# Optimization experiments

Hardware: AMD Instinct MI355X
Metric: run time of the kernel (lower is better)

Reference implementation:

```python
import jax, jax.numpy as jnp
import numpy as np

EMBED_DIM = 512
NUM_HEADS = 8
WINDOW = 5
OVERLAP = 1
STRIDE = WINDOW - OVERLAP  # 4


def setup_inputs() -> dict:
    key = jax.random.key(0)
    ks = jax.random.split(key, 5)
    B, S, D = 8, 4096, EMBED_DIM
    s = 1.0 / np.sqrt(D).astype(np.float32)
    return {
        "x": jax.random.normal(ks[0], (B, S, D), jnp.float32),
        "Wq": jax.random.normal(ks[1], (D, D), jnp.float32) * s,
        "bq": jnp.zeros((D,), jnp.float32),
        "Wk": jax.random.normal(ks[2], (D, D), jnp.float32) * s,
        "bk": jnp.zeros((D,), jnp.float32),
        "Wv": jax.random.normal(ks[3], (D, D), jnp.float32) * s,
        "bv": jnp.zeros((D,), jnp.float32),
        "Wo": jax.random.normal(ks[4], (D, D), jnp.float32) * s,
        "bo": jnp.zeros((D,), jnp.float32),
    }


def reference(x, Wq, bq, Wk, bk, Wv, bv, Wo, bo):
    B, S, D = x.shape
    H = NUM_HEADS
    hd = D // H
    pad = (WINDOW - S % WINDOW) % WINDOW
    xp = jnp.pad(x, ((0, 0), (0, pad), (0, 0)))
    P = S + pad
    nw = (P - WINDOW) // STRIDE + 1

    # gather all sliding windows at once: [B, nw, W, D]
    idx = (jnp.arange(nw) * STRIDE)[:, None] + jnp.arange(WINDOW)  # [nw, W]
    win = xp[:, idx]

    def proj(t, W, b):
        return (t @ W + b).reshape(B, nw, WINDOW, H, hd)

    q = proj(win, Wq, bq)
    k = proj(win, Wk, bk)
    v = proj(win, Wv, bv)

    scale = jnp.float32(1.0 / np.sqrt(hd))
    scores = jnp.einsum('bnqhd,bnkhd->bnhqk', q, k) * scale  # [B,nw,H,W,W]
    attn = jax.nn.softmax(scores, axis=-1)
    o = jnp.einsum('bnhqk,bnkhd->bnqhd', attn, v).reshape(B, nw, WINDOW, D)
    o = o @ Wo + bo  # window outputs [B,nw,W,D]

    # overlap-add + count-average (exactly as the torch loop does)
    flat_idx = idx.reshape(-1)
    out = jnp.zeros((B, P, D), jnp.float32).at[:, flat_idx].add(
        o.reshape(B, nw * WINDOW, D))
    counts = jnp.zeros((P,), jnp.float32).at[flat_idx].add(1.0)
    out = out / (counts[None, :, None] + 1e-6)
    out = out[:, :S]

    # torch: sum(all_weights) / num_windows  -> mean over window axis
    attn_weights = attn.mean(axis=1)  # [B, H, W, W]
    return out, attn_weights
```

## Files before the change

kernel.cpp:

```cpp
#include <hip/hip_runtime.h>
#include <hip/hip_bf16.h>


#define SEQ   4096
#define NB    8
#define DIM   512
#define NWIN  1024
#define MTOT  (NB*SEQ)

typedef __bf16 bf16x8 __attribute__((ext_vector_type(8)));
typedef float  f32x4  __attribute__((ext_vector_type(4)));

__device__ __forceinline__ float b2f(unsigned short u) {
  union { unsigned int i; float f; } z; z.i = ((unsigned int)u) << 16; return z.f;
}
__device__ __forceinline__ unsigned short f2b(float f) {
  __bf16 h = (__bf16)f; return __builtin_bit_cast(unsigned short, h);
}
__device__ __forceinline__ void gload_lds16(const void* g, void* l) {
  __builtin_amdgcn_global_load_lds(
      (__attribute__((address_space(1))) void*)g,
      (__attribute__((address_space(3))) void*)l, 16, 0, 0);
}

#define FENCE() asm volatile("" ::: "memory")
#define BAR()   __builtin_amdgcn_s_barrier()
#define LGK0()  asm volatile("s_waitcnt lgkmcnt(0)" ::: "memory")
#define SCHB()  __builtin_amdgcn_sched_barrier(0)
#define VMW4()  asm volatile("s_waitcnt vmcnt(4)" ::: "memory")
#define VMW0()  asm volatile("s_waitcnt vmcnt(0)" ::: "memory")

__global__ __launch_bounds__(256) void cvt_x(const float* __restrict__ x,
                                             unsigned short* __restrict__ o, int n8) {
  int stride = gridDim.x * blockDim.x;
  for (int i = blockIdx.x * blockDim.x + threadIdx.x; i < n8; i += stride) {
    const float4 a = *(const float4*)(x + (size_t)i * 8);
    const float4 c = *(const float4*)(x + (size_t)i * 8 + 4);
    unsigned short u[8] = {f2b(a.x), f2b(a.y), f2b(a.z), f2b(a.w),
                           f2b(c.x), f2b(c.y), f2b(c.z), f2b(c.w)};
    *(int4*)(o + (size_t)i * 8) = *(const int4*)u;
  }
}

__global__ __launch_bounds__(256) void cvt_w(const float* __restrict__ W0, const float* __restrict__ W1,
                                             const float* __restrict__ W2, const float* __restrict__ W3,
                                             unsigned short* __restrict__ Wt) {
  int i = blockIdx.x * 256 + threadIdx.x;
  int w = i >> 18;
  int r = i & 262143;
  int nn = r >> 9, kk = r & 511;
  const float* W = (w == 0) ? W0 : (w == 1) ? W1 : (w == 2) ? W2 : W3;
  Wt[i] = f2b(W[kk * 512 + nn]);
}

__device__ __forceinline__ void stage_part(int h, const unsigned short* pa, const unsigned short* pb,
    int r0s, int c0s, int r1s, int c1s, char* ldsb, int wid) {
  int kt = h >> 2, slot = (h + 2) & 3;
  int buf = kt & 1, ab = slot >> 1, half = slot & 1;
  const unsigned short* src = ab ? pb : pa;
  int rb = half << 7;
  int kc = kt << 6;
  char* d = ldsb + buf * 65536 + ab * 32768 + half * 16384 + wid * 1024;
  gload_lds16(src + (size_t)(rb + r0s) * 512 + kc + c0s, d);
  gload_lds16(src + (size_t)(rb + r1s) * 512 + kc + c1s, d + 8192);
}

#define LDSB(off) (*(const bf16x8*)(ldsb + (off)))

#define RA4(BUF, HALF) { \
  _Pragma("unroll") for (int mf2 = 0; mf2 < 4; ++mf2) { \
    _Pragma("unroll") for (int ks = 0; ks < 2; ++ks) \
      a[mf2][ks] = LDSB(aS[BUF][ks] + (HALF) * 8192 + mf2 * 2048); } }

#define RB2(BUF, QN) { \
  _Pragma("unroll") for (int nf2 = 0; nf2 < 2; ++nf2) { \
    _Pragma("unroll") for (int ks = 0; ks < 2; ++ks) \
      b[(QN)*2+nf2][ks] = LDSB(bS[BUF][ks] + (QN) * 4096 + nf2 * 2048); } }

#define MMQ(QM, QN) { \
  _Pragma("unroll") for (int ks = 0; ks < 2; ++ks) \
  _Pragma("unroll") for (int mf2 = 0; mf2 < 4; ++mf2) \
  _Pragma("unroll") for (int nf2 = 0; nf2 < 2; ++nf2) \
    acc[(QM)*4+mf2][(QN)*2+nf2] = __builtin_amdgcn_mfma_f32_16x16x32_bf16( \
      a[mf2][ks], b[(QN)*2+nf2][ks], acc[(QM)*4+mf2][(QN)*2+nf2], 0, 0, 0); }

template<int MODE>
__global__ __launch_bounds__(512, 2) void gemm8(
    const unsigned short* __restrict__ A, const unsigned short* __restrict__ Bw,
    const float* __restrict__ b0, const float* __restrict__ b1, const float* __restrict__ b2,
    unsigned short* __restrict__ o0, unsigned short* __restrict__ o1, unsigned short* __restrict__ o2,
    float* __restrict__ fout) {
  __shared__ unsigned short lds_[65536];
  char* ldsb = (char*)lds_;

  const int nwg = gridDim.x;
  const int cpx = nwg >> 3;
  const int g = blockIdx.x;
  const int sw = (g & 7) * cpx + (g >> 3);
  constexpr int NTN = (MODE == 0) ? 6 : 2;
  const int ntile = sw % NTN, mtile = sw / NTN;
  const int m0 = mtile * 256, n0g = ntile * 256;

  const int tid = threadIdx.x;
  const int lane = tid & 63;
  const int wid = tid >> 6;
  const int wr = wid >> 2, wc = wid & 3;
  const int cl16 = lane & 15, hi = lane >> 4;
  const int hi16 = hi * 16;
  const int sxor = (cl16 & 14) << 3;

  int o0_ = tid * 16;
  int o1_ = 8192 + tid * 16;
  int l0 = o0_ ^ (((o0_ >> 8) & 7) << 4);
  int l1 = o1_ ^ (((o1_ >> 8) & 7) << 4);
  const int r0s = l0 >> 7, c0s = (l0 & 127) >> 1;
  const int r1s = l1 >> 7, c1s = (l1 & 127) >> 1;

  const unsigned short* pa = A + (size_t)m0 * 512;
  const unsigned short* pb = Bw + (size_t)n0g * 512;

  int aS[2][2], bS[2][2];
#pragma unroll
  for (int bu = 0; bu < 2; ++bu)
#pragma unroll
    for (int ks = 0; ks < 2; ++ks) {
      aS[bu][ks] = bu * 65536 + ((wr * 16384 + cl16 * 128 + ks * 64 + hi16) ^ sxor);
      bS[bu][ks] = bu * 65536 + 32768 + (((wc >> 1) * 16384 + (wc & 1) * 8192 + cl16 * 128 + ks * 64 + hi16) ^ sxor);
    }

  f32x4 acc[8][4] = {};
  bf16x8 a[4][2], b[4][2];

#define STG(H) stage_part((H), pa, pb, r0s, c0s, r1s, c1s, ldsb, wid)

  STG(0); STG(1); STG(2); STG(3); STG(4); STG(5);
  VMW4();
  FENCE(); BAR();

#pragma unroll
  for (int it = 0; it < 4; ++it) {
    const int hb = 8 * it;
    RA4(0, 0); RB2(0, 0);
    STG(hb + 6);
    FENCE(); BAR(); LGK0(); SCHB();
    __builtin_amdgcn_s_setprio(1); MMQ(0, 0); __builtin_amdgcn_s_setprio(0);
    FENCE(); BAR();
    RB2(0, 1);
    if (hb + 7 < 32) STG(hb + 7);
    FENCE(); BAR(); LGK0(); SCHB();
    __builtin_amdgcn_s_setprio(1); MMQ(0, 1); __builtin_amdgcn_s_setprio(0);
    FENCE(); BAR();
    RA4(0, 1);
    if (it < 3) STG(hb + 8);
    FENCE(); BAR(); LGK0(); SCHB();
    __builtin_amdgcn_s_setprio(1); MMQ(1, 1); __builtin_amdgcn_s_setprio(0);
    FENCE(); BAR();
    if (it < 3) STG(hb + 9);
    FENCE(); BAR();
    __builtin_amdgcn_s_setprio(1); MMQ(1, 0); __builtin_amdgcn_s_setprio(0);
    if (it < 3) { VMW4(); } else { VMW0(); }
    FENCE(); BAR();
    RA4(1, 0); RB2(1, 0);
    if (it < 3) STG(hb + 10);
    FENCE(); BAR(); LGK0(); SCHB();
    __builtin_amdgcn_s_setprio(1); MMQ(0, 0); __builtin_amdgcn_s_setprio(0);
    FENCE(); BAR();
    RB2(1, 1);
    if (it < 3) STG(hb + 11);
    FENCE(); BAR(); LGK0(); SCHB();
    __builtin_amdgcn_s_setprio(1); MMQ(0, 1); __builtin_amdgcn_s_setprio(0);
    FENCE(); BAR();
    RA4(1, 1);
    if (it < 3) STG(hb + 12);
    FENCE(); BAR(); LGK0(); SCHB();
    __builtin_amdgcn_s_setprio(1); MMQ(1, 1); __builtin_amdgcn_s_setprio(0);
    FENCE(); BAR();
    if (it < 3) STG(hb + 13);
    FENCE(); BAR();
    __builtin_amdgcn_s_setprio(1); MMQ(1, 0); __builtin_amdgcn_s_setprio(0);
    if (it < 3) { VMW4(); }
    FENCE(); BAR();
  }

  if constexpr (MODE == 0) {
    const int sel = n0g >> 9;
    const float* bias = (sel == 0) ? b0 : (sel == 1) ? b1 : b2;
    unsigned short* C = (sel == 0) ? o0 : (sel == 1) ? o1 : o2;
    const int lcb = (n0g & 511) + wc * 64;
    unsigned short* wlds = lds_ + wid * 8192;
#pragma unroll
    for (int mf = 0; mf < 8; ++mf)
#pragma unroll
      for (int nf = 0; nf < 4; ++nf) {
        float bv_ = bias[lcb + nf * 16 + cl16];
#pragma unroll
        for (int r = 0; r < 4; ++r) {
          int w = (mf * 16 + hi * 4 + r) * 64 + nf * 16 + cl16;
          wlds[w ^ (((w >> 7) & 7) << 3)] = f2b(acc[mf][nf][r] + bv_);
        }
      }
    LGK0();
#pragma unroll
    for (int itr = 0; itr < 16; ++itr) {
      int f = itr * 512 + lane * 8;
      int row = f >> 6, col = f & 63;
      int4 v = *(const int4*)&wlds[f ^ (((f >> 7) & 7) << 3)];
      *(int4*)(C + (size_t)(m0 + wr * 128 + row) * 512 + lcb + col) = v;
    }
  } else {
#pragma unroll
    for (int nf = 0; nf < 4; ++nf) {
      int ncol = n0g + wc * 64 + nf * 16 + cl16;
      float bv_ = b0[ncol];
#pragma unroll
      for (int mf = 0; mf < 8; ++mf) {
        int rbase = m0 + wr * 128 + mf * 16 + hi * 4;
#pragma unroll
        for (int r = 0; r < 4; ++r) {
          int row = rbase + r;
          int s = row & (SEQ - 1);
          float cnt = ((s & 3) == 0 && s > 0) ? 2.0f : 1.0f;
          fout[(size_t)row * 512 + ncol] = (acc[mf][nf][r] + cnt * bv_) / (cnt + 1e-6f);
        }
      }
    }
  }
}

__global__ __launch_bounds__(256) void attn_win(
    const unsigned short* __restrict__ Qb, const unsigned short* __restrict__ Kb,
    const unsigned short* __restrict__ Vb,
    const float* __restrict__ bq, const float* __restrict__ bk, const float* __restrict__ bv,
    unsigned short* __restrict__ yb, unsigned short* __restrict__ yext,
    float* __restrict__ abuf) {
  const int gw = blockIdx.x * 4 + (threadIdx.x >> 6);
  const int b = gw >> 10, n = gw & (NWIN - 1);
  const int lane = threadIdx.x & 63;
  const int h = lane >> 3, e = lane & 7;
  const int dbase = h * 64 + e * 8;

  float kf[5][8], vf[5][8];
#pragma unroll
  for (int j = 0; j < 5; ++j) {
    int p = 4 * n + j;
    if (p < SEQ) {
      int4 kv = *(const int4*)(Kb + ((size_t)b * SEQ + p) * DIM + dbase);
      int4 vv = *(const int4*)(Vb + ((size_t)b * SEQ + p) * DIM + dbase);
      const unsigned short* kp = (const unsigned short*)&kv;
      const unsigned short* vp = (const unsigned short*)&vv;
#pragma unroll
      for (int d = 0; d < 8; ++d) { kf[j][d] = b2f(kp[d]); vf[j][d] = b2f(vp[d]); }
    } else {
#pragma unroll
      for (int d = 0; d < 8; ++d) { kf[j][d] = bk[dbase + d]; vf[j][d] = bv[dbase + d]; }
    }
  }
  float pm[5][5];
#pragma unroll
  for (int i = 0; i < 5; ++i) {
    int p = 4 * n + i;
    float qf[8];
    if (p < SEQ) {
      int4 qv = *(const int4*)(Qb + ((size_t)b * SEQ + p) * DIM + dbase);
      const unsigned short* qp = (const unsigned short*)&qv;
#pragma unroll
      for (int d = 0; d < 8; ++d) qf[d] = b2f(qp[d]);
    } else {
#pragma unroll
      for (int d = 0; d < 8; ++d) qf[d] = bq[dbase + d];
    }
    float sr[5];
#pragma unroll
    for (int j = 0; j < 5; ++j) {
      float t = 0.f;
#pragma unroll
      for (int d = 0; d < 8; ++d) t += qf[d] * kf[j][d];
      t += __shfl_xor(t, 1);
      t += __shfl_xor(t, 2);
      t += __shfl_xor(t, 4);
      sr[j] = t * 0.125f;
    }
    float mx = sr[0];
#pragma unroll
    for (int j = 1; j < 5; ++j) mx = fmaxf(mx, sr[j]);
    float ex[5], sum = 0.f;
#pragma unroll
    for (int j = 0; j < 5; ++j) { ex[j] = expf(sr[j] - mx); sum += ex[j]; }
    float inv = 1.0f / sum;
#pragma unroll
    for (int j = 0; j < 5; ++j) pm[i][j] = ex[j] * inv;
    float o[8];
#pragma unroll
    for (int d = 0; d < 8; ++d) o[d] = 0.f;
#pragma unroll
    for (int j = 0; j < 5; ++j)
#pragma unroll
      for (int d = 0; d < 8; ++d) o[d] += pm[i][j] * vf[j][d];
    unsigned short u[8];
#pragma unroll
    for (int d = 0; d < 8; ++d) u[d] = f2b(o[d]);
    if (i < 4) {
      *(int4*)(yb + ((size_t)b * SEQ + p) * DIM + dbase) = *(const int4*)u;
    } else {
      *(int4*)(yext + ((size_t)b * NWIN + n) * DIM + dbase) = *(const int4*)u;
    }
  }
  float* ap = abuf + ((size_t)(b * NWIN + n) * 8 + h) * 25;
  if (e == 0) {
#pragma unroll
    for (int i2 = 0; i2 < 5; ++i2)
#pragma unroll
      for (int j2 = 0; j2 < 5; ++j2) ap[i2 * 5 + j2] = pm[i2][j2];
  }
}

__global__ __launch_bounds__(256) void merge_y(unsigned short* __restrict__ y,
                                               const unsigned short* __restrict__ ye) {
  int idx = blockIdx.x * 256 + threadIdx.x;
  if (idx >= 8 * 1023 * 64) return;
  int d8 = idx & 63;
  int t = idx >> 6;
  int n = t % 1023 + 1;
  int b = t / 1023;
  size_t yo = ((size_t)b * SEQ + 4 * (size_t)n) * DIM + d8 * 8;
  size_t eo = ((size_t)b * NWIN + (n - 1)) * DIM + d8 * 8;
  int4 av = *(const int4*)(y + yo);
  int4 cv = *(const int4*)(ye + eo);
  const unsigned short* ap = (const unsigned short*)&av;
  const unsigned short* cp = (const unsigned short*)&cv;
  unsigned short u[8];
#pragma unroll
  for (int j = 0; j < 8; ++j) u[j] = f2b(b2f(ap[j]) + b2f(cp[j]));
  *(int4*)(y + yo) = *(const int4*)u;
}

__global__ __launch_bounds__(256) void attn_reduce(const float* __restrict__ abuf,
                                                   float* __restrict__ out) {
  __shared__ float sm[256][25];
  int bh = blockIdx.x;
  int b = bh >> 3, h = bh & 7;
  int t = threadIdx.x;
  float loc[25];
#pragma unroll
  for (int j = 0; j < 25; ++j) loc[j] = 0.f;
  for (int n = t; n < NWIN; n += 256) {
    const float* p = abuf + ((size_t)(b * NWIN + n) * 8 + h) * 25;
#pragma unroll
    for (int j = 0; j < 25; ++j) loc[j] += p[j];
  }
#pragma unroll
  for (int j = 0; j < 25; ++j) sm[t][j] = loc[j];
  __syncthreads();
  for (int off = 128; off > 0; off >>= 1) {
    if (t < off)
#pragma unroll
      for (int j = 0; j < 25; ++j) sm[t][j] += sm[t + off][j];
    __syncthreads();
  }
  if (t < 25) out[bh * 25 + t] = sm[0][t] * (1.0f / 1024.0f);
}

extern "C" void kernel_launch(void* const* d_in, const int* in_sizes, int n_in,
                              void* d_out, int out_size, void* d_ws, size_t ws_size,
                              hipStream_t stream) {
  const float* x  = (const float*)d_in[0];
  const float* Wq = (const float*)d_in[1];
  const float* bq = (const float*)d_in[2];
  const float* Wk = (const float*)d_in[3];
  const float* bk = (const float*)d_in[4];
  const float* Wv = (const float*)d_in[5];
  const float* bv = (const float*)d_in[6];
  const float* Wo = (const float*)d_in[7];
  const float* bo = (const float*)d_in[8];
  float* out = (float*)d_out;

  char* ws = (char*)d_ws;
  unsigned short* xb   = (unsigned short*)(ws);
  unsigned short* yb   = xb;
  unsigned short* Qb   = (unsigned short*)(ws + 33554432);
  unsigned short* Kb   = (unsigned short*)(ws + 67108864);
  unsigned short* Vb   = (unsigned short*)(ws + 100663296);
  unsigned short* yext = (unsigned short*)(ws + 134217728);
  float*          abuf = (float*)(ws + 142606336);
  unsigned short* Wt   = (unsigned short*)(ws + 149159936);
  (void)ws_size; (void)in_sizes; (void)n_in; (void)out_size;

  cvt_x<<<2048, 256, 0, stream>>>(x, xb, MTOT * DIM / 8);
  cvt_w<<<4096, 256, 0, stream>>>(Wq, Wk, Wv, Wo, Wt);
  gemm8<0><<<768, 512, 0, stream>>>(xb, Wt, bq, bk, bv, Qb, Kb, Vb, nullptr);
  attn_win<<<2048, 256, 0, stream>>>(Qb, Kb, Vb, bq, bk, bv, yb, yext, abuf);
  merge_y<<<2046, 256, 0, stream>>>(yb, yext);
  gemm8<1><<<256, 512, 0, stream>>>(yb, Wt + 3 * (DIM * DIM), bo, nullptr, nullptr,
                                    nullptr, nullptr, nullptr, out);
  attn_reduce<<<64, 256, 0, stream>>>(abuf, out + (size_t)MTOT * DIM);
}
```

Before: 160.1 us.

## Replace 8-phase interleaved GEMM schedule with simple double-buffered k-tile pipeline

The GEMM main loop used a fine-grained 8-phase schedule that interleaved quarter-tile staging, LDS reads, MFMA bursts, priority bumps and many barriers. It is replaced by a plain two-buffer loop: prefetch the whole next k-tile (four stage parts), wait on vmcnt, barrier, then do all LDS reads and MFMAs for the current buffer. This drops most barriers, sched_barriers and setprio calls to cut synchronisation overhead and simplify scheduling. In exchange it gives up the finer overlap between global loads, LDS reads and MFMA work that the old schedule tried to provide.

Measured after the change: 166.7 us. 1.04x slower.

```diff
diff --git a/kernel.cpp b/kernel.cpp
--- a/kernel.cpp
+++ b/kernel.cpp
@@ -25,10 +25,9 @@
 
 #define FENCE() asm volatile("" ::: "memory")
 #define BAR()   __builtin_amdgcn_s_barrier()
+#define VMW8()  asm volatile("s_waitcnt vmcnt(8)" ::: "memory")
+#define VMW0()  asm volatile("s_waitcnt vmcnt(0)" ::: "memory")
 #define LGK0()  asm volatile("s_waitcnt lgkmcnt(0)" ::: "memory")
-#define SCHB()  __builtin_amdgcn_sched_barrier(0)
-#define VMW4()  asm volatile("s_waitcnt vmcnt(4)" ::: "memory")
-#define VMW0()  asm volatile("s_waitcnt vmcnt(0)" ::: "memory")
 
 __global__ __launch_bounds__(256) void cvt_x(const float* __restrict__ x,
                                              unsigned short* __restrict__ o, int n8) {
@@ -85,7 +84,7 @@
       a[mf2][ks], b[(QN)*2+nf2][ks], acc[(QM)*4+mf2][(QN)*2+nf2], 0, 0, 0); }
 
 template<int MODE>
-__global__ __launch_bounds__(512, 2) void gemm8(
+__global__ __launch_bounds__(512, 2) void gemm2p(
     const unsigned short* __restrict__ A, const unsigned short* __restrict__ Bw,
     const float* __restrict__ b0, const float* __restrict__ b1, const float* __restrict__ b2,
     unsigned short* __restrict__ o0, unsigned short* __restrict__ o1, unsigned short* __restrict__ o2,
@@ -131,55 +130,24 @@
   f32x4 acc[8][4] = {};
   bf16x8 a[4][2], b[4][2];
 
-#define STG(H) stage_part((H), pa, pb, r0s, c0s, r1s, c1s, ldsb, wid)
-
-  STG(0); STG(1); STG(2); STG(3); STG(4); STG(5);
-  VMW4();
-  FENCE(); BAR();
-
-#pragma unroll
-  for (int it = 0; it < 4; ++it) {
-    const int hb = 8 * it;
-    RA4(0, 0); RB2(0, 0);
-    STG(hb + 6);
-    FENCE(); BAR(); LGK0(); SCHB();
-    __builtin_amdgcn_s_setprio(1); MMQ(0, 0); __builtin_amdgcn_s_setprio(0);
-    FENCE(); BAR();
-    RB2(0, 1);
-    if (hb + 7 < 32) STG(hb + 7);
-    FENCE(); BAR(); LGK0(); SCHB();
-    __builtin_amdgcn_s_setprio(1); MMQ(0, 1); __builtin_amdgcn_s_setprio(0);
-    FENCE(); BAR();
-    RA4(0, 1);
-    if (it < 3) STG(hb + 8);
-    FENCE(); BAR(); LGK0(); SCHB();
-    __builtin_amdgcn_s_setprio(1); MMQ(1, 1); __builtin_amdgcn_s_setprio(0);
-    FENCE(); BAR();
-    if (it < 3) STG(hb + 9);
-    FENCE(); BAR();
-    __builtin_amdgcn_s_setprio(1); MMQ(1, 0); __builtin_amdgcn_s_setprio(0);
-    if (it < 3) { VMW4(); } else { VMW0(); }
-    FENCE(); BAR();
-    RA4(1, 0); RB2(1, 0);
-    if (it < 3) STG(hb + 10);
-    FENCE(); BAR(); LGK0(); SCHB();
-    __builtin_amdgcn_s_setprio(1); MMQ(0, 0); __builtin_amdgcn_s_setprio(0);
-    FENCE(); BAR();
-    RB2(1, 1);
-    if (it < 3) STG(hb + 11);
-    FENCE(); BAR(); LGK0(); SCHB();
-    __builtin_amdgcn_s_setprio(1); MMQ(0, 1); __builtin_amdgcn_s_setprio(0);
-    FENCE(); BAR();
-    RA4(1, 1);
-    if (it < 3) STG(hb + 12);
-    FENCE(); BAR(); LGK0(); SCHB();
-    __builtin_amdgcn_s_setprio(1); MMQ(1, 1); __builtin_amdgcn_s_setprio(0);
-    FENCE(); BAR();
-    if (it < 3) STG(hb + 13);
-    FENCE(); BAR();
-    __builtin_amdgcn_s_setprio(1); MMQ(1, 0); __builtin_amdgcn_s_setprio(0);
-    if (it < 3) { VMW4(); }
-    FENCE(); BAR();
+#define STG4(KT) { stage_part((KT)*4, pa, pb, r0s, c0s, r1s, c1s, ldsb, wid); \
+                   stage_part((KT)*4+1, pa, pb, r0s, c0s, r1s, c1s, ldsb, wid); \
+                   stage_part((KT)*4+2, pa, pb, r0s, c0s, r1s, c1s, ldsb, wid); \
+                   stage_part((KT)*4+3, pa, pb, r0s, c0s, r1s, c1s, ldsb, wid); }
+
+  STG4(0);
+
+#pragma unroll
+  for (int kt = 0; kt < 8; ++kt) {
+    const int bu = kt & 1;
+    if (kt < 7) { STG4(kt + 1); VMW8(); } else { VMW0(); }
+    FENCE(); BAR(); FENCE();
+    RB2(bu, 0); RB2(bu, 1);
+    RA4(bu, 0);
+    MMQ(0, 0); MMQ(0, 1);
+    RA4(bu, 1);
+    MMQ(1, 1); MMQ(1, 0);
+    FENCE(); BAR(); FENCE();
   }
 
   if constexpr (MODE == 0) {
@@ -387,10 +355,10 @@
 
   cvt_x<<<2048, 256, 0, stream>>>(x, xb, MTOT * DIM / 8);
   cvt_w<<<4096, 256, 0, stream>>>(Wq, Wk, Wv, Wo, Wt);
-  gemm8<0><<<768, 512, 0, stream>>>(xb, Wt, bq, bk, bv, Qb, Kb, Vb, nullptr);
+  gemm2p<0><<<768, 512, 0, stream>>>(xb, Wt, bq, bk, bv, Qb, Kb, Vb, nullptr);
   attn_win<<<2048, 256, 0, stream>>>(Qb, Kb, Vb, bq, bk, bv, yb, yext, abuf);
   merge_y<<<2046, 256, 0, stream>>>(yb, yext);
-  gemm8<1><<<256, 512, 0, stream>>>(yb, Wt + 3 * (DIM * DIM), bo, nullptr, nullptr,
-                                    nullptr, nullptr, nullptr, out);
+  gemm2p<1><<<256, 512, 0, stream>>>(yb, Wt + 3 * (DIM * DIM), bo, nullptr, nullptr,
+                                     nullptr, nullptr, nullptr, out);
   attn_reduce<<<64, 256, 0, stream>>>(abuf, out + (size_t)MTOT * DIM);
 }
```

## Fuse overlap merge into a new output-projection GEMM and relax QKV GEMM waits

Applied to the files above, without the earlier changes.

Drops the separate merge_y pass. A new 128x128-tile gemm_final kernel adds the extra-window rows (yext) into the A operand while loading it, then applies the bias and count-average epilogue. This removes one full read-modify-write pass over the activations and one kernel launch. The tuned gemm8 MODE 1 path is replaced by a simpler register-staged, double-read kernel that may use the tensor cores less efficiently. Separately, the explicit lgkmcnt(0) waits and sched_barriers are removed from the QKV GEMM loop so the compiler can schedule the LDS reads and MFMAs itself.

Measured after the change: 198.7 us. +24.1%, slower.

```diff
diff --git a/kernel.cpp b/kernel.cpp
--- a/kernel.cpp
+++ b/kernel.cpp
@@ -26,7 +26,6 @@
 #define FENCE() asm volatile("" ::: "memory")
 #define BAR()   __builtin_amdgcn_s_barrier()
 #define LGK0()  asm volatile("s_waitcnt lgkmcnt(0)" ::: "memory")
-#define SCHB()  __builtin_amdgcn_sched_barrier(0)
 #define VMW4()  asm volatile("s_waitcnt vmcnt(4)" ::: "memory")
 #define VMW0()  asm volatile("s_waitcnt vmcnt(0)" ::: "memory")
 
@@ -88,8 +87,7 @@
 __global__ __launch_bounds__(512, 2) void gemm8(
     const unsigned short* __restrict__ A, const unsigned short* __restrict__ Bw,
     const float* __restrict__ b0, const float* __restrict__ b1, const float* __restrict__ b2,
-    unsigned short* __restrict__ o0, unsigned short* __restrict__ o1, unsigned short* __restrict__ o2,
-    float* __restrict__ fout) {
+    unsigned short* __restrict__ o0, unsigned short* __restrict__ o1, unsigned short* __restrict__ o2) {
   __shared__ unsigned short lds_[65536];
   char* ldsb = (char*)lds_;
 
@@ -97,7 +95,7 @@
   const int cpx = nwg >> 3;
   const int g = blockIdx.x;
   const int sw = (g & 7) * cpx + (g >> 3);
-  constexpr int NTN = (MODE == 0) ? 6 : 2;
+  constexpr int NTN = 6;
   const int ntile = sw % NTN, mtile = sw / NTN;
   const int m0 = mtile * 256, n0g = ntile * 256;
 
@@ -142,17 +140,17 @@
     const int hb = 8 * it;
     RA4(0, 0); RB2(0, 0);
     STG(hb + 6);
-    FENCE(); BAR(); LGK0(); SCHB();
+    FENCE(); BAR();
     __builtin_amdgcn_s_setprio(1); MMQ(0, 0); __builtin_amdgcn_s_setprio(0);
     FENCE(); BAR();
     RB2(0, 1);
     if (hb + 7 < 32) STG(hb + 7);
-    FENCE(); BAR(); LGK0(); SCHB();
+    FENCE(); BAR();
     __builtin_amdgcn_s_setprio(1); MMQ(0, 1); __builtin_amdgcn_s_setprio(0);
     FENCE(); BAR();
     RA4(0, 1);
     if (it < 3) STG(hb + 8);
-    FENCE(); BAR(); LGK0(); SCHB();
+    FENCE(); BAR();
     __builtin_amdgcn_s_setprio(1); MMQ(1, 1); __builtin_amdgcn_s_setprio(0);
     FENCE(); BAR();
     if (it < 3) STG(hb + 9);
@@ -162,17 +160,17 @@
     FENCE(); BAR();
     RA4(1, 0); RB2(1, 0);
     if (it < 3) STG(hb + 10);
-    FENCE(); BAR(); LGK0(); SCHB();
+    FENCE(); BAR();
     __builtin_amdgcn_s_setprio(1); MMQ(0, 0); __builtin_amdgcn_s_setprio(0);
     FENCE(); BAR();
     RB2(1, 1);
     if (it < 3) STG(hb + 11);
-    FENCE(); BAR(); LGK0(); SCHB();
+    FENCE(); BAR();
     __builtin_amdgcn_s_setprio(1); MMQ(0, 1); __builtin_amdgcn_s_setprio(0);
     FENCE(); BAR();
     RA4(1, 1);
     if (it < 3) STG(hb + 12);
-    FENCE(); BAR(); LGK0(); SCHB();
+    FENCE(); BAR();
     __builtin_amdgcn_s_setprio(1); MMQ(1, 1); __builtin_amdgcn_s_setprio(0);
     FENCE(); BAR();
     if (it < 3) STG(hb + 13);
@@ -182,7 +180,7 @@
     FENCE(); BAR();
   }
 
-  if constexpr (MODE == 0) {
+  {
     const int sel = n0g >> 9;
     const float* bias = (sel == 0) ? b0 : (sel == 1) ? b1 : b2;
     unsigned short* C = (sel == 0) ? o0 : (sel == 1) ? o1 : o2;
@@ -206,23 +204,6 @@
       int row = f >> 6, col = f & 63;
       int4 v = *(const int4*)&wlds[f ^ (((f >> 7) & 7) << 3)];
       *(int4*)(C + (size_t)(m0 + wr * 128 + row) * 512 + lcb + col) = v;
-    }
-  } else {
-#pragma unroll
-    for (int nf = 0; nf < 4; ++nf) {
-      int ncol = n0g + wc * 64 + nf * 16 + cl16;
-      float bv_ = b0[ncol];
-#pragma unroll
-      for (int mf = 0; mf < 8; ++mf) {
-        int rbase = m0 + wr * 128 + mf * 16 + hi * 4;
-#pragma unroll
-        for (int r = 0; r < 4; ++r) {
-          int row = rbase + r;
-          int s = row & (SEQ - 1);
-          float cnt = ((s & 3) == 0 && s > 0) ? 2.0f : 1.0f;
-          fout[(size_t)row * 512 + ncol] = (acc[mf][nf][r] + cnt * bv_) / (cnt + 1e-6f);
-        }
-      }
     }
   }
 }
@@ -314,24 +295,98 @@
   }
 }
 
-__global__ __launch_bounds__(256) void merge_y(unsigned short* __restrict__ y,
-                                               const unsigned short* __restrict__ ye) {
-  int idx = blockIdx.x * 256 + threadIdx.x;
-  if (idx >= 8 * 1023 * 64) return;
-  int d8 = idx & 63;
-  int t = idx >> 6;
-  int n = t % 1023 + 1;
-  int b = t / 1023;
-  size_t yo = ((size_t)b * SEQ + 4 * (size_t)n) * DIM + d8 * 8;
-  size_t eo = ((size_t)b * NWIN + (n - 1)) * DIM + d8 * 8;
-  int4 av = *(const int4*)(y + yo);
-  int4 cv = *(const int4*)(ye + eo);
-  const unsigned short* ap = (const unsigned short*)&av;
-  const unsigned short* cp = (const unsigned short*)&cv;
-  unsigned short u[8];
-#pragma unroll
-  for (int j = 0; j < 8; ++j) u[j] = f2b(b2f(ap[j]) + b2f(cp[j]));
-  *(int4*)(y + yo) = *(const int4*)u;
+__device__ __forceinline__ void load_final_stage(
+    const unsigned short* __restrict__ Yb, const unsigned short* __restrict__ Yext,
+    const unsigned short* __restrict__ Bt, int m0, int n0, int k0, int tid,
+    int4* av, int4* bv) {
+#pragma unroll
+  for (int it = 0; it < 2; ++it) {
+    int c = it * 256 + tid;
+    int row = c >> 2, kk = (c & 3) << 3;
+    bv[it] = *(const int4*)(Bt + (size_t)(n0 + row) * 512 + k0 + kk);
+    int gr = m0 + row;
+    int4 v = *(const int4*)(Yb + (size_t)gr * 512 + k0 + kk);
+    int s = gr & (SEQ - 1);
+    if ((s & 3) == 0 && s > 0) {
+      int b = gr >> 12;
+      int4 ev = *(const int4*)(Yext + ((size_t)b * NWIN + (s >> 2) - 1) * 512 + k0 + kk);
+      unsigned short* pv = (unsigned short*)&v;
+      const unsigned short* pe = (const unsigned short*)&ev;
+#pragma unroll
+      for (int j = 0; j < 8; ++j) pv[j] = f2b(b2f(pv[j]) + b2f(pe[j]));
+    }
+    av[it] = v;
+  }
+}
+
+__global__ __launch_bounds__(256) void gemm_final(
+    const unsigned short* __restrict__ Yb, const unsigned short* __restrict__ Yext,
+    const unsigned short* __restrict__ Bt, const float* __restrict__ bo,
+    float* __restrict__ Cout) {
+  __shared__ unsigned short As[128 * 40];
+  __shared__ unsigned short Bs[128 * 40];
+  const int g = blockIdx.x;
+  const int sw = (g & 7) * 128 + (g >> 3);
+  const int ntile = sw & 3, mtile = sw >> 2;
+  const int m0 = mtile * 128, n0 = ntile * 128;
+
+  const int tid = threadIdx.x;
+  const int lane = tid & 63;
+  const int wid = tid >> 6;
+  const int wr = wid >> 1, wc = wid & 1;
+  const int cl = lane & 15, hi8 = (lane >> 4) << 3;
+
+  f32x4 acc[4][4] = {};
+  int4 av[2], bv[2];
+  load_final_stage(Yb, Yext, Bt, m0, n0, 0, tid, av, bv);
+
+  for (int k0 = 0; k0 < 512; k0 += 32) {
+#pragma unroll
+    for (int it = 0; it < 2; ++it) {
+      int c = it * 256 + tid;
+      int row = c >> 2, kk = (c & 3) << 3;
+      *(int4*)&As[row * 40 + kk] = av[it];
+      *(int4*)&Bs[row * 40 + kk] = bv[it];
+    }
+    if (k0 + 32 < 512)
+      load_final_stage(Yb, Yext, Bt, m0, n0, k0 + 32, tid, av, bv);
+    __syncthreads();
+    bf16x8 af[4], bfr[4];
+#pragma unroll
+    for (int m = 0; m < 4; ++m) {
+      int r = wr * 64 + m * 16 + cl;
+      af[m] = __builtin_bit_cast(bf16x8, *(const int4*)&As[r * 40 + hi8]);
+    }
+#pragma unroll
+    for (int n = 0; n < 4; ++n) {
+      int r = wc * 64 + n * 16 + cl;
+      bfr[n] = __builtin_bit_cast(bf16x8, *(const int4*)&Bs[r * 40 + hi8]);
+    }
+#pragma unroll
+    for (int m = 0; m < 4; ++m)
+#pragma unroll
+      for (int n = 0; n < 4; ++n)
+        acc[m][n] = __builtin_amdgcn_mfma_f32_16x16x32_bf16(af[m], bfr[n], acc[m][n], 0, 0, 0);
+    __syncthreads();
+  }
+
+  const int rh = lane >> 4;
+#pragma unroll
+  for (int n = 0; n < 4; ++n) {
+    int col = n0 + wc * 64 + n * 16 + cl;
+    float bcol = bo[col];
+#pragma unroll
+    for (int m = 0; m < 4; ++m) {
+      int rbase = m0 + wr * 64 + m * 16 + rh * 4;
+#pragma unroll
+      for (int r = 0; r < 4; ++r) {
+        int row = rbase + r;
+        int s = row & (SEQ - 1);
+        float cnt = ((s & 3) == 0 && s > 0) ? 2.0f : 1.0f;
+        Cout[(size_t)row * 512 + col] = (acc[m][n][r] + cnt * bcol) / (cnt + 1e-6f);
+      }
+    }
+  }
 }
 
 __global__ __launch_bounds__(256) void attn_reduce(const float* __restrict__ abuf,
@@ -387,10 +442,8 @@
 
   cvt_x<<<2048, 256, 0, stream>>>(x, xb, MTOT * DIM / 8);
   cvt_w<<<4096, 256, 0, stream>>>(Wq, Wk, Wv, Wo, Wt);
-  gemm8<0><<<768, 512, 0, stream>>>(xb, Wt, bq, bk, bv, Qb, Kb, Vb, nullptr);
+  gemm8<0><<<768, 512, 0, stream>>>(xb, Wt, bq, bk, bv, Qb, Kb, Vb);
   attn_win<<<2048, 256, 0, stream>>>(Qb, Kb, Vb, bq, bk, bv, yb, yext, abuf);
-  merge_y<<<2046, 256, 0, stream>>>(yb, yext);
-  gemm8<1><<<256, 512, 0, stream>>>(yb, Wt + 3 * (DIM * DIM), bo, nullptr, nullptr,
-                                    nullptr, nullptr, nullptr, out);
+  gemm_final<<<1024, 256, 0, stream>>>(yb, yext, Wt + 3 * (DIM * DIM), bo, out);
   attn_reduce<<<64, 256, 0, stream>>>(abuf, out + (size_t)MTOT * DIM);
 }
```
